# Kernel tuning notes

Measured on AMD Instinct MI355X. Metric: run time of the kernel, lower is better.

The kernel has to match this reference:

```python
import jax, jax.numpy as jnp
import numpy as np

B = 16
TOP_N = 4
IOU_THRESH = 0.25
PAD = 224
OUT = 224  # part image size
NUM_CLASSES = 200


def _gen_anchors(input_shape=(448, 448)):
    # Faithful port of NTSNet._generate_default_anchor_maps -> edge anchors,
    # then +PAD shift and int cast as in NTSNet.__init__.
    scales = [2.0 ** (1.0 / 3.0), 2.0 ** (2.0 / 3.0)]
    ratios = [0.667, 1.0, 1.5]
    settings = [(32, 48, scales), (64, 96, scales), (128, 192, [1.0] + scales)]
    edge = []
    for stride, size, scs in settings:
        H = int(np.ceil(input_shape[0] / stride))
        W = int(np.ceil(input_shape[1] / stride))
        ostart = stride / 2.0
        oy = np.arange(ostart, ostart + stride * H, stride).reshape(H, 1)
        ox = np.arange(ostart, ostart + stride * W, stride).reshape(1, W)
        cy = np.broadcast_to(oy, (H, W)).astype(np.float32)
        cx = np.broadcast_to(ox, (H, W)).astype(np.float32)
        for s in scs:
            for ar in ratios:
                h = size * s / float(ar) ** 0.5
                w = size * s * float(ar) ** 0.5
                e = np.stack([cy - h / 2.0, cx - w / 2.0, cy + h / 2.0, cx + w / 2.0], axis=-1)
                edge.append(e.reshape(-1, 4))
    edge = np.concatenate(edge, axis=0).astype(np.float32)
    return (edge + PAD).astype(np.int64).astype(np.int32)  # [1614,4] (y0,x0,y1,x1)


def _conv(x, w, b, stride, pad):
    y = jax.lax.conv_general_dilated(
        x, w, window_strides=(stride, stride),
        padding=[(pad, pad), (pad, pad)],
        dimension_numbers=("NCHW", "OIHW", "NCHW"))
    return y + b[None, :, None, None]


def _nms_single(scores, boxes, areas):
    # Hard NMS, fixed TOP_N iterations (jit-friendly): iteratively take the
    # highest-score box and suppress boxes with IoU >= IOU_THRESH.
    valid = jnp.ones(scores.shape, dtype=bool)
    picked = []
    for _ in range(TOP_N):
        i = jnp.argmax(jnp.where(valid, scores, -jnp.inf))
        b = boxes[i]
        ih = jnp.minimum(boxes[:, 2], b[2]) - jnp.maximum(boxes[:, 0], b[0])
        iw = jnp.minimum(boxes[:, 3], b[3]) - jnp.maximum(boxes[:, 1], b[1])
        inter = jnp.where((ih < 0) | (iw < 0), 0.0, ih * iw)
        iou = inter / (areas + areas[i] - inter)
        valid = valid & (iou < IOU_THRESH)
        picked.append(i)
    return jnp.stack(picked)  # [TOP_N]


def _crop_resize(img, box):
    # Bilinear resize of img[:, y0:y1, x0:x1] to OUTxOUT, align_corners=True
    # (matches F.interpolate(..., mode='bilinear', align_corners=True)).
    y0, x0, y1, x1 = box[0], box[1], box[2], box[3]
    h = (y1 - y0).astype(jnp.float32)
    w = (x1 - x0).astype(jnp.float32)
    t = jnp.arange(OUT, dtype=jnp.float32)
    sy = t * (h - 1.0) / (OUT - 1.0)
    sx = t * (w - 1.0) / (OUT - 1.0)
    fy = jnp.floor(sy)
    fx = jnp.floor(sx)
    wy = (sy - fy)[None, :, None]  # broadcast over rows
    wx = (sx - fx)[None, None, :]  # broadcast over cols
    iy0 = y0 + fy.astype(jnp.int32)
    ix0 = x0 + fx.astype(jnp.int32)
    iy1 = jnp.minimum(iy0 + 1, y1 - 1)
    ix1 = jnp.minimum(ix0 + 1, x1 - 1)
    r0 = img[:, iy0]  # [3,OUT,896]
    r1 = img[:, iy1]
    top = r0[:, :, ix0] * (1.0 - wx) + r0[:, :, ix1] * wx
    bot = r1[:, :, ix0] * (1.0 - wx) + r1[:, :, ix1] * wx
    return top * (1.0 - wy) + bot * wy  # [3,OUT,OUT]


def setup_inputs() -> dict:
    key = jax.random.key(0)
    ks = jax.random.split(key, 10)
    s = 0.02
    inp = {
        "x": jax.random.normal(ks[0], (B, 3, 448, 448), jnp.float32),
        "bb_w": jax.random.normal(ks[1], (2048, 3, 32, 32), jnp.float32) * s,
        "bb_b": jnp.zeros((2048,), jnp.float32),
        "n1_dw": jax.random.normal(ks[2], (128, 2048, 3, 3), jnp.float32) * s,
        "n1_db": jnp.zeros((128,), jnp.float32),
        "n1_tw": jax.random.normal(ks[3], (6, 128, 1, 1), jnp.float32) * s,
        "n1_tb": jnp.zeros((6,), jnp.float32),
        "n2_dw": jax.random.normal(ks[4], (128, 128, 3, 3), jnp.float32) * s,
        "n2_db": jnp.zeros((128,), jnp.float32),
        "n2_tw": jax.random.normal(ks[5], (6, 128, 1, 1), jnp.float32) * s,
        "n2_tb": jnp.zeros((6,), jnp.float32),
        "n3_dw": jax.random.normal(ks[6], (128, 128, 3, 3), jnp.float32) * s,
        "n3_db": jnp.zeros((128,), jnp.float32),
        "n3_tw": jax.random.normal(ks[7], (9, 128, 1, 1), jnp.float32) * s,
        "n3_tb": jnp.zeros((9,), jnp.float32),
        "cn_w": jax.random.normal(ks[8], (NUM_CLASSES, 10240), jnp.float32) * s,
        "cn_b": jnp.zeros((NUM_CLASSES,), jnp.float32),
        "anchors": jnp.asarray(_gen_anchors()),
    }
    return inp


def reference(x, bb_w, bb_b, n1_dw, n1_db, n1_tw, n1_tb, n2_dw, n2_db, n2_tw,
              n2_tb, n3_dw, n3_db, n3_tw, n3_tb, cn_w, cn_b, anchors):
    batch = x.shape[0]
    # Backbone -> raw pre-features [B,2048,14,14]
    raw = _conv(x, bb_w, bb_b, stride=32, pad=0)
    # Navigator unit -> rpn scores [B,1614]
    y1 = jax.nn.relu(_conv(raw, n1_dw, n1_db, 1, 1))            # [B,128,14,14]
    t1 = _conv(y1, n1_tw, n1_tb, 1, 0).reshape(batch, -1)        # [B,1176]
    y2 = jax.nn.relu(_conv(y1, n2_dw, n2_db, 2, 1))              # [B,128,7,7]
    t2 = _conv(y2, n2_tw, n2_tb, 1, 0).reshape(batch, -1)        # [B,294]
    y3 = jax.nn.relu(_conv(y2, n3_dw, n3_db, 2, 1))              # [B,128,4,4]
    t3 = _conv(y3, n3_tw, n3_tb, 1, 0).reshape(batch, -1)        # [B,144]
    rpn_score = jnp.concatenate([t1, t2, t3], axis=1)            # [B,1614]

    boxes_f = anchors.astype(jnp.float32)
    areas = (boxes_f[:, 2] - boxes_f[:, 0]) * (boxes_f[:, 3] - boxes_f[:, 1])
    top_idx = jax.vmap(_nms_single, in_axes=(0, None, None))(rpn_score, boxes_f, areas)  # [B,TOP_N]

    x_pad = jnp.pad(x, ((0, 0), (0, 0), (PAD, PAD), (PAD, PAD)))  # [B,3,896,896]
    sel_boxes = anchors[top_idx]                                  # [B,TOP_N,4]
    part_imgs = jax.vmap(lambda img, bs: jax.vmap(_crop_resize, in_axes=(None, 0))(img, bs))(
        x_pad, sel_boxes)                                         # [B,TOP_N,3,224,224]
    part_imgs = jax.lax.stop_gradient(part_imgs).reshape(batch * TOP_N, 3, OUT, OUT)

    # Shared backbone + tail (global avg pool; dropout is identity in eval)
    part_features = _conv(part_imgs, bb_w, bb_b, 32, 0).mean(axis=(2, 3))  # [B*TOP_N,2048]
    part_feature = part_features.reshape(batch, TOP_N, -1)[:, :4].reshape(batch, -1)  # num_cat=4
    raw_features = jax.lax.stop_gradient(raw).mean(axis=(2, 3))            # [B,2048]

    concat_out = jnp.concatenate([part_feature, raw_features], axis=1)     # [B,10240]
    concat_logits = concat_out @ cn_w.T + cn_b
    return concat_logits
```

## Files before the change

### kernel.cpp

```cpp
#include <hip/hip_runtime.h>
#include <cstdint>
#include <math.h>

typedef _Float16 half_t;
typedef __attribute__((ext_vector_type(8))) _Float16 half8;
typedef __attribute__((ext_vector_type(4))) float floatx4;


typedef __attribute__((address_space(3))) unsigned int lds_u32;
typedef const __attribute__((address_space(1))) unsigned int glb_u32;
__device__ __forceinline__ void glds16(const void* g, void* l) {
    __builtin_amdgcn_global_load_lds((glb_u32*)g, (lds_u32*)l, 16, 0, 0);
}

__global__ __launch_bounds__(256)
void prep_all(const float* __restrict__ x, const float* __restrict__ bbw,
              const float* __restrict__ n1dw, const float* __restrict__ n2dw,
              const float* __restrict__ n3dw, const float* __restrict__ cnb,
              const float* __restrict__ bbb,
              half_t* __restrict__ xh,
              half_t* __restrict__ bh, half_t* __restrict__ w1h,
              float* __restrict__ wt2t, float* __restrict__ wt3t,
              float* __restrict__ out, float* __restrict__ zpad,
              float* __restrict__ concat)
{
    const long t = (long)blockIdx.x * 256 + threadIdx.x;
    if (t < 1228800) {
        const int m = (int)(t % 3200), k8 = (int)(t / 3200);
        const int mt = m >> 7, mr = m & 127, s = k8 >> 2, kg = k8 & 3;
        const size_t dst = (((size_t)(mt * 96 + s) * 4 + kg) * 128 + mr) * 8;
        float f[8];
        if (m < 3136) {
            const int bq = m / 196, pos = m % 196, oy = pos / 14, ox = pos % 14;
            const int k = k8 * 8, c = k >> 10, r = (k >> 5) & 31, cc = k & 31;
            const float* p = x + ((size_t)(bq * 3 + c) * 448 + oy * 32 + r) * 448 + ox * 32 + cc;
            *(float4*)&f[0] = *(const float4*)p;
            *(float4*)&f[4] = *(const float4*)(p + 4);
        } else {
            #pragma unroll
            for (int j = 0; j < 8; ++j) f[j] = 0.f;
        }
        half8 h;
        #pragma unroll
        for (int j = 0; j < 8; ++j) h[j] = (half_t)f[j];
        *(half8*)(xh + dst) = h;
    } else if (t < 2015232) {
        const int t2 = (int)(t - 1228800);
        const int n = t2 / 384, k8 = t2 % 384;
        const float* p = bbw + (size_t)n * 3072 + k8 * 8;
        float f[8];
        *(float4*)&f[0] = *(const float4*)p;
        *(float4*)&f[4] = *(const float4*)(p + 4);
        const int nt = n >> 6, nr = n & 63, s = k8 >> 2, kg = k8 & 3;
        const size_t dst = (((size_t)(nt * 96 + s) * 4 + kg) * 64 + nr) * 8;
        half8 h;
        #pragma unroll
        for (int j = 0; j < 8; ++j) h[j] = (half_t)f[j];
        *(half8*)(bh + dst) = h;
    } else if (t < 2048000) {
        const int t2 = (int)(t - 2015232);
        const int n = t2 >> 8, ic8 = t2 & 255;
        const int s = ic8 >> 2, kg = ic8 & 3;
        const float* src = n1dw + ((size_t)n * 2048 + ic8 * 8) * 9;
        float buf[72];
        #pragma unroll
        for (int i = 0; i < 18; ++i) *(float4*)&buf[i * 4] = *(const float4*)(src + i * 4);
        #pragma unroll
        for (int tap = 0; tap < 9; ++tap) {
            half8 h;
            #pragma unroll
            for (int j = 0; j < 8; ++j) h[j] = (half_t)buf[j * 9 + tap];
            const size_t dst = (((size_t)(tap * 64 + s) * 4 + kg) * 128 + n) * 8;
            *(half8*)(w1h + dst) = h;
        }
    } else if (t < 2195456) {
        const int t2 = (int)(t - 2048000);
        const int oc = t2 % 128, rest = t2 / 128, ic = rest % 128, tap = rest / 128;
        wt2t[(tap * 128 + ic) * 128 + oc] = n2dw[((size_t)oc * 128 + ic) * 9 + tap];
    } else if (t < 2342912) {
        const int t2 = (int)(t - 2195456);
        const int oc = t2 % 128, rest = t2 / 128, ic = rest % 128, tap = rest / 128;
        wt3t[(tap * 128 + ic) * 128 + oc] = n3dw[((size_t)oc * 128 + ic) * 9 + tap];
    } else if (t < 2346112) {
        const int i = (int)(t - 2342912);
        out[i] = cnb[i % 200];
    } else if (t < 2346368) {
        zpad[t - 2346112] = 0.f;
    } else if (t < 2510208) {
        const int i = (int)(t - 2346368);
        const int r = i % 10240;
        concat[i] = (r < 8192) ? bbb[r & 2047] : 0.f;
    }
}

__global__ __launch_bounds__(256)
void gemm_x(const half_t* __restrict__ Ah, const half_t* __restrict__ Bh,
            const float* __restrict__ bias, half_t* __restrict__ outh)
{
    __shared__ __align__(16) char L[24576];
    const int tid = threadIdx.x, lane = tid & 63, wv = tid >> 6;
    const int nt = blockIdx.x, mt = blockIdx.y;
    const int lm = lane & 15, quad = lane >> 4;

    const char* gA = (const char*)Ah + (size_t)(mt >> 1) * 786432 + (mt & 1) * 1024 + lane * 16;
    const char* gB = (const char*)Bh + (size_t)(2 * nt) * 393216 + lane * 16;

    const int a0 = 2 * wv, a1 = 2 * wv + 1;
    const int aof0 = (a0 >> 2) * 4096 + (a0 & 3) * 1024;
    const int aog0 = (a0 >> 2) * 8192 + (a0 & 3) * 2048;
    const int aof1 = (a1 >> 2) * 4096 + (a1 & 3) * 1024;
    const int aog1 = (a1 >> 2) * 8192 + (a1 & 3) * 2048;
    const int bsi = wv >> 1, bnh = wv & 1;
    const size_t bgb = (size_t)bnh * 393216 + bsi * 4096;
    const int blb = 8192 + (bsi * 2 + bnh) * 4096;

    floatx4 acc[8];
    const floatx4 fz = {0.f, 0.f, 0.f, 0.f};
    #pragma unroll
    for (int j = 0; j < 8; ++j) acc[j] = fz;

    for (int s = 0; s < 48; ++s) {
        const size_t sa = (size_t)(2 * s) * 8192;
        const size_t sb = (size_t)(2 * s) * 4096;
        glds16(gA + sa + aog0, L + aof0);
        glds16(gA + sa + aog1, L + aof1);
        #pragma unroll
        for (int i = 0; i < 4; ++i)
            glds16(gB + bgb + sb + i * 1024, L + blb + i * 1024);
        __syncthreads();
        #pragma unroll
        for (int ki = 0; ki < 2; ++ki) {
            half8 a = *(const half8*)(L + ki * 4096 + quad * 1024 + (wv * 16 + lm) * 16);
            #pragma unroll
            for (int j = 0; j < 8; ++j) {
                half8 b = *(const half8*)(L + 8192 + (ki * 2 + (j >> 2)) * 4096 + quad * 1024 + ((j & 3) * 16 + lm) * 16);
                acc[j] = __builtin_amdgcn_mfma_f32_16x16x32_f16(a, b, acc[j], 0, 0, 0);
            }
        }
        __syncthreads();
    }
    const int m0 = mt * 64 + wv * 16 + quad * 4;
    #pragma unroll
    for (int j = 0; j < 8; ++j) {
        const int n = nt * 128 + j * 16 + lm;
        const float bv = bias[n];
        #pragma unroll
        for (int r = 0; r < 4; ++r)
            outh[(size_t)(m0 + r) * 2048 + n] = (half_t)(acc[j][r] + bv);
    }
}

__global__ __launch_bounds__(256)
void gemm_nav(const half_t* __restrict__ rawh, const half_t* __restrict__ Bh,
              const char* __restrict__ zpad, float* __restrict__ y1p)
{
    __shared__ __align__(16) char L[24576];
    const int tid = threadIdx.x, lane = tid & 63, wv = tid >> 6;
    const int tx = blockIdx.x;
    const int tap = tx >> 1, ks = tx & 1;
    const int mt = blockIdx.y;
    const int lm = lane & 15, quad = lane >> 4;

    const int grow = mt * 64 + lane;
    const int b = grow / 196, pos = grow % 196, oy = pos / 14, ox = pos % 14;
    const int iy = oy + tap / 3 - 1, ix = ox + tap % 3 - 1;
    const bool av = (iy >= 0 && iy < 14 && ix >= 0 && ix < 14);
    const char* abase = av ? (const char*)rawh + ((size_t)(b * 196 + iy * 14 + ix)) * 4096 + ks * 2048 : zpad;
    const int stp = av ? 1 : 0;

    const int a0 = 2 * wv, a1 = 2 * wv + 1;
    const int ac0 = (a0 >> 2) * 64 + (a0 & 3) * 16, al0 = (a0 >> 2) * 4096 + (a0 & 3) * 1024;
    const int ac1 = (a1 >> 2) * 64 + (a1 & 3) * 16, al1 = (a1 >> 2) * 4096 + (a1 & 3) * 1024;
    const int bsi = wv >> 1, bnh = wv & 1;
    const char* gB = (const char*)Bh + (size_t)tap * 524288 + (size_t)(ks * 32) * 8192 + bnh * 1024 + lane * 16;
    const int blb = 8192 + bsi * 8192 + bnh * 1024;

    floatx4 acc[8];
    const floatx4 fz = {0.f, 0.f, 0.f, 0.f};
    #pragma unroll
    for (int j = 0; j < 8; ++j) acc[j] = fz;

    for (int s = 0; s < 16; ++s) {
        const int rowo = s * 128;
        glds16(abase + stp * (rowo + ac0), L + al0);
        glds16(abase + stp * (rowo + ac1), L + al1);
        const size_t sb = (size_t)(2 * s + bsi) * 8192;
        #pragma unroll
        for (int i = 0; i < 4; ++i)
            glds16(gB + sb + i * 2048, L + blb + i * 2048);
        __syncthreads();
        #pragma unroll
        for (int ki = 0; ki < 2; ++ki) {
            half8 a = *(const half8*)(L + ki * 4096 + quad * 1024 + (wv * 16 + lm) * 16);
            #pragma unroll
            for (int j = 0; j < 8; ++j) {
                half8 bq = *(const half8*)(L + 8192 + ki * 8192 + quad * 2048 + (j * 16 + lm) * 16);
                acc[j] = __builtin_amdgcn_mfma_f32_16x16x32_f16(a, bq, acc[j], 0, 0, 0);
            }
        }
        __syncthreads();
    }
    const int m0 = mt * 64 + wv * 16 + quad * 4;
    #pragma unroll
    for (int j = 0; j < 8; ++j) {
        const int n = j * 16 + lm;
        #pragma unroll
        for (int r = 0; r < 4; ++r)
            y1p[((size_t)tx * 3136 + m0 + r) * 128 + n] = acc[j][r];
    }
}

__global__ __launch_bounds__(256)
void y1r_rm(const float* __restrict__ y1p, const float* __restrict__ bias,
            float* __restrict__ y1,
            const half_t* __restrict__ rh, float* __restrict__ concat)
{
    if (blockIdx.x < 1568) {
        const int t = blockIdx.x * 256 + threadIdx.x;
        const int n = t & 127;
        float s = bias[n];
        #pragma unroll
        for (int ks = 0; ks < 18; ++ks) s += y1p[(size_t)ks * 3136 * 128 + t];
        y1[t] = fmaxf(s, 0.f);
    } else {
        const int t = (blockIdx.x - 1568) * 256 + threadIdx.x;
        const int n = t & 2047, b = (t >> 11) & 15, pc = t >> 15;
        float s = 0.f;
        const int p0 = pc * 49;
        for (int p = p0; p < p0 + 49; ++p)
            s += (float)rh[(size_t)(b * 196 + p) * 2048 + n];
        atomicAdd(concat + (size_t)b * 10240 + 8192 + n, s * (1.f / 196.f));
    }
}

__device__ __forceinline__ void tidy_one(const float* in, const float* wr, float bi,
                                         float* dst, int lane)
{
    float acc = in[lane] * wr[lane] + in[lane + 64] * wr[lane + 64];
    #pragma unroll
    for (int s = 32; s > 0; s >>= 1) acc += __shfl_down(acc, s, 64);
    if (lane == 0) *dst = acc + bi;
}

__device__ __forceinline__ void conv_s2_body(int t, const float* __restrict__ in,
                                             const float* __restrict__ wt,
                                             const float* __restrict__ bias,
                                             float* __restrict__ out, int Win, int Wout)
{
    const int oc = t & 127;
    const int pos = (t >> 7) % (Wout * Wout);
    const int b = t / (128 * Wout * Wout);
    if (b >= 16) return;
    const int oy = pos / Wout, ox = pos % Wout;
    float acc = bias[oc];
    for (int dy = 0; dy < 3; ++dy) {
        const int y = oy * 2 + dy - 1;
        if (y < 0 || y >= Win) continue;
        for (int dx = 0; dx < 3; ++dx) {
            const int x = ox * 2 + dx - 1;
            if (x < 0 || x >= Win) continue;
            const float* ip = in + (size_t)(b * Win * Win + y * Win + x) * 128;
            const float* wp = wt + (size_t)(dy * 3 + dx) * 16384 + oc;
            for (int ic = 0; ic < 128; ++ic)
                acc += ip[ic] * wp[ic * 128];
        }
    }
    out[(size_t)(b * Wout * Wout + pos) * 128 + oc] = fmaxf(acc, 0.f);
}

__global__ __launch_bounds__(256)
void conv2_tidy1(const float* __restrict__ y1, const float* __restrict__ wt2t,
                 const float* __restrict__ b2d, float* __restrict__ y2,
                 const float* __restrict__ w1t, const float* __restrict__ b1t,
                 float* __restrict__ scores)
{
    if (blockIdx.x < 392) {
        conv_s2_body(blockIdx.x * 256 + threadIdx.x, y1, wt2t, b2d, y2, 14, 7);
    } else {
        const int wid = (blockIdx.x - 392) * 4 + (threadIdx.x >> 6);
        const int lane = threadIdx.x & 63;
        if (wid >= 16 * 1176) return;
        const int b = wid / 1176, i1 = wid % 1176;
        const int ch = i1 / 196, pos = i1 % 196;
        tidy_one(y1 + (size_t)(b * 196 + pos) * 128, w1t + ch * 128, b1t[ch],
                 scores + b * 1614 + i1, lane);
    }
}

__global__ __launch_bounds__(256)
void conv3_tidy2(const float* __restrict__ y2, const float* __restrict__ wt3t,
                 const float* __restrict__ b3d, float* __restrict__ y3,
                 const float* __restrict__ w2t, const float* __restrict__ b2t,
                 float* __restrict__ scores)
{
    if (blockIdx.x < 128) {
        conv_s2_body(blockIdx.x * 256 + threadIdx.x, y2, wt3t, b3d, y3, 7, 4);
    } else {
        const int wid = (blockIdx.x - 128) * 4 + (threadIdx.x >> 6);
        const int lane = threadIdx.x & 63;
        if (wid >= 16 * 294) return;
        const int b = wid / 294, i2 = wid % 294;
        const int ch = i2 / 49, pos = i2 % 49;
        tidy_one(y2 + (size_t)(b * 49 + pos) * 128, w2t + ch * 128, b2t[ch],
                 scores + b * 1614 + 1176 + i2, lane);
    }
}

__global__ __launch_bounds__(256)
void tidy3(const float* __restrict__ y3, const float* __restrict__ w3t,
           const float* __restrict__ b3t, float* __restrict__ scores)
{
    const int wid = blockIdx.x * 4 + (threadIdx.x >> 6);
    const int lane = threadIdx.x & 63;
    if (wid >= 16 * 144) return;
    const int b = wid / 144, i3 = wid % 144;
    const int ch = i3 / 16, pos = i3 % 16;
    tidy_one(y3 + (size_t)(b * 16 + pos) * 128, w3t + ch * 128, b3t[ch],
             scores + b * 1614 + 1470 + i3, lane);
}

__global__ __launch_bounds__(256)
void nms(const float* __restrict__ scores, const int* __restrict__ anchors,
         int* __restrict__ top_idx)
{
    __shared__ float wv_v[4];
    __shared__ int wv_i[4];
    __shared__ int s_pick;
    const int b = blockIdx.x, tid = threadIdx.x;
    const int lane = tid & 63, wv = tid >> 6;
    float sc[7], ay0[7], ax0[7], ay1[7], ax1[7];
    unsigned int vmask = 0;
    #pragma unroll
    for (int j = 0; j < 7; ++j) {
        const int i = tid + j * 256;
        if (i < 1614) {
            sc[j]  = scores[b * 1614 + i];
            ay0[j] = (float)anchors[i * 4 + 0];
            ax0[j] = (float)anchors[i * 4 + 1];
            ay1[j] = (float)anchors[i * 4 + 2];
            ax1[j] = (float)anchors[i * 4 + 3];
            vmask |= 1u << j;
        }
    }
    for (int r = 0; r < 4; ++r) {
        float bv = -INFINITY; int bi = 0x7fffffff;
        #pragma unroll
        for (int j = 0; j < 7; ++j) {
            if (vmask & (1u << j)) {
                const float v = sc[j];
                const int i = tid + j * 256;
                if (v > bv || (v == bv && i < bi)) { bv = v; bi = i; }
            }
        }
        #pragma unroll
        for (int s = 32; s > 0; s >>= 1) {
            const float v2 = __shfl_down(bv, s, 64);
            const int   i2 = __shfl_down(bi, s, 64);
            if (v2 > bv || (v2 == bv && i2 < bi)) { bv = v2; bi = i2; }
        }
        if (lane == 0) { wv_v[wv] = bv; wv_i[wv] = bi; }
        __syncthreads();
        if (tid == 0) {
            float fv = wv_v[0]; int fi = wv_i[0];
            #pragma unroll
            for (int k = 1; k < 4; ++k)
                if (wv_v[k] > fv || (wv_v[k] == fv && wv_i[k] < fi)) { fv = wv_v[k]; fi = wv_i[k]; }
            s_pick = fi;
            top_idx[b * 4 + r] = fi;
        }
        __syncthreads();
        const int pick = s_pick;
        const float py0 = (float)anchors[pick * 4 + 0], px0 = (float)anchors[pick * 4 + 1];
        const float py1 = (float)anchors[pick * 4 + 2], px1 = (float)anchors[pick * 4 + 3];
        const float pa = (py1 - py0) * (px1 - px0);
        #pragma unroll
        for (int j = 0; j < 7; ++j) {
            if (vmask & (1u << j)) {
                const float ih = fminf(ay1[j], py1) - fmaxf(ay0[j], py0);
                const float iw = fminf(ax1[j], px1) - fmaxf(ax0[j], px0);
                const float inter = (ih < 0.f || iw < 0.f) ? 0.f : ih * iw;
                const float area = (ay1[j] - ay0[j]) * (ax1[j] - ax0[j]);
                const float iou = inter / ((area + pa) - inter);
                if (iou >= 0.25f) vmask &= ~(1u << j);
            }
        }
    }
}

__global__ __launch_bounds__(256)
void crop_mean(const float* __restrict__ x, const int* __restrict__ anchors,
               const int* __restrict__ top_idx, float* __restrict__ abar)
{
    __shared__ float red[256];
    const int bi = blockIdx.x;
    const int q = bi / 96, rem = bi % 96, c = rem >> 5, r = rem & 31;
    const int tid = threadIdx.x;
    const int cc = tid & 31, ps = tid >> 5;
    const int idx = top_idx[q];
    const int y0 = anchors[idx * 4 + 0], x0 = anchors[idx * 4 + 1];
    const int y1 = anchors[idx * 4 + 2], x1 = anchors[idx * 4 + 3];
    const float hh = (float)(y1 - y0), ww = (float)(x1 - x0);
    const float* xb = x + (size_t)((q >> 2) * 3 + c) * 200704;
    float acc = 0.f;
    for (int p = ps; p < 49; p += 8) {
        const int oy = p / 7, ox = p % 7;
        const int typ = oy * 32 + r;
        const int txp = ox * 32 + cc;
        const float sy = (float)typ * (hh - 1.0f) / 223.0f;
        const float fy = floorf(sy);
        const float wy = sy - fy;
        const int iy0 = y0 + (int)fy;
        const int iy1 = min(iy0 + 1, y1 - 1);
        const float sx = (float)txp * (ww - 1.0f) / 223.0f;
        const float fx = floorf(sx);
        const float wx = sx - fx;
        const int ix0 = x0 + (int)fx;
        const int ix1 = min(ix0 + 1, x1 - 1);
        const int ry0 = iy0 - 224, ry1 = iy1 - 224;
        const int rx0 = ix0 - 224, rx1 = ix1 - 224;
        const bool vy0 = (ry0 >= 0 && ry0 < 448), vy1 = (ry1 >= 0 && ry1 < 448);
        const bool vx0 = (rx0 >= 0 && rx0 < 448), vx1 = (rx1 >= 0 && rx1 < 448);
        const float v00 = (vy0 && vx0) ? xb[(size_t)ry0 * 448 + rx0] : 0.f;
        const float v01 = (vy0 && vx1) ? xb[(size_t)ry0 * 448 + rx1] : 0.f;
        const float v10 = (vy1 && vx0) ? xb[(size_t)ry1 * 448 + rx0] : 0.f;
        const float v11 = (vy1 && vx1) ? xb[(size_t)ry1 * 448 + rx1] : 0.f;
        const float top = v00 * (1.f - wx) + v01 * wx;
        const float bot = v10 * (1.f - wx) + v11 * wx;
        acc += top * (1.f - wy) + bot * wy;
    }
    red[tid] = acc;
    __syncthreads();
    if (tid < 32) {
        float s = 0.f;
        #pragma unroll
        for (int k = 0; k < 8; ++k) s += red[tid + 32 * k];
        abar[(size_t)q * 3072 + c * 1024 + r * 32 + cc] = s * (1.f / 49.f);
    }
}

__global__ __launch_bounds__(256)
void part_gemm(const float* __restrict__ abar, const half_t* __restrict__ Bh,
               float* __restrict__ concat)
{
    __shared__ __align__(16) char L[12288];
    const int tid = threadIdx.x, lane = tid & 63, wv = tid >> 6;
    const int lm = lane & 15, quad = lane >> 4;
    const int nt = blockIdx.x, ks = blockIdx.y;
    const char* gBh = (const char*)Bh + ((size_t)nt * 96 + ks * 12) * 4096 + lane * 16;
    const int am = tid & 63, akg = tid >> 6;

    floatx4 acc[4], accl[4];
    const floatx4 fz = {0.f, 0.f, 0.f, 0.f};
    #pragma unroll
    for (int j = 0; j < 4; ++j) { acc[j] = fz; accl[j] = fz; }

    for (int s = 0; s < 12; ++s) {
        {
            const float* pa = abar + (size_t)am * 3072 + (ks * 12 + s) * 32 + akg * 8;
            float f[8];
            *(float4*)&f[0] = *(const float4*)pa;
            *(float4*)&f[4] = *(const float4*)(pa + 4);
            half8 h, l;
            #pragma unroll
            for (int j = 0; j < 8; ++j) {
                const half_t hh = (half_t)f[j];
                h[j] = hh;
                l[j] = (half_t)(f[j] - (float)hh);
            }
            *(half8*)(L + (akg * 64 + am) * 16) = h;
            *(half8*)(L + 4096 + (akg * 64 + am) * 16) = l;
        }
        glds16(gBh + (size_t)s * 4096 + wv * 1024, L + 8192 + wv * 1024);
        __syncthreads();
        half8 ah, al, bh[4];
        ah = *(const half8*)(L + (quad * 64 + wv * 16 + lm) * 16);
        al = *(const half8*)(L + 4096 + (quad * 64 + wv * 16 + lm) * 16);
        #pragma unroll
        for (int j = 0; j < 4; ++j) bh[j] = *(const half8*)(L + 8192 + (quad * 64 + j * 16 + lm) * 16);
        #pragma unroll
        for (int j = 0; j < 4; ++j) {
            acc[j]  = __builtin_amdgcn_mfma_f32_16x16x32_f16(ah, bh[j], acc[j], 0, 0, 0);
            accl[j] = __builtin_amdgcn_mfma_f32_16x16x32_f16(al, bh[j], accl[j], 0, 0, 0);
        }
        __syncthreads();
    }
    #pragma unroll
    for (int j = 0; j < 4; ++j) {
        const int n = nt * 64 + j * 16 + lm;
        #pragma unroll
        for (int r = 0; r < 4; ++r) {
            const int m = wv * 16 + quad * 4 + r;
            atomicAdd(concat + (size_t)(m >> 2) * 10240 + (m & 3) * 2048 + n,
                      acc[j][r] + accl[j][r]);
        }
    }
}

__global__ __launch_bounds__(256)
void cls_gemm(const float* __restrict__ concat, const float* __restrict__ w,
              float* __restrict__ out)
{
    __shared__ float ws_[8 * 321];
    __shared__ float cs_[16 * 321];
    __shared__ float red[256];
    const int nchunk = blockIdx.x, ks = blockIdx.y;
    const int tid = threadIdx.x;
    for (int i = tid; i < 2560; i += 256) {
        const int r = i / 320, k = i % 320;
        ws_[r * 321 + k] = w[(size_t)(nchunk * 8 + r) * 10240 + ks * 320 + k];
    }
    for (int i = tid; i < 5120; i += 256) {
        const int r = i / 320, k = i % 320;
        cs_[r * 321 + k] = concat[(size_t)r * 10240 + ks * 320 + k];
    }
    __syncthreads();
    const int b = tid & 15, c = (tid >> 4) & 7, hf = tid >> 7;
    const float* cp = cs_ + b * 321 + hf * 160;
    const float* wp = ws_ + c * 321 + hf * 160;
    float a = 0.f;
    #pragma unroll 8
    for (int k = 0; k < 160; ++k) a += cp[k] * wp[k];
    red[tid] = a;
    __syncthreads();
    if (tid < 128) atomicAdd(out + b * 200 + nchunk * 8 + c, red[tid] + red[tid + 128]);
}

extern "C" void kernel_launch(void* const* d_in, const int* in_sizes, int n_in,
                              void* d_out, int out_size, void* d_ws, size_t ws_size,
                              hipStream_t stream)
{
    const float* x     = (const float*)d_in[0];
    const float* bb_w  = (const float*)d_in[1];
    const float* bb_b  = (const float*)d_in[2];
    const float* n1_dw = (const float*)d_in[3];
    const float* n1_db = (const float*)d_in[4];
    const float* n1_tw = (const float*)d_in[5];
    const float* n1_tb = (const float*)d_in[6];
    const float* n2_dw = (const float*)d_in[7];
    const float* n2_db = (const float*)d_in[8];
    const float* n2_tw = (const float*)d_in[9];
    const float* n2_tb = (const float*)d_in[10];
    const float* n3_dw = (const float*)d_in[11];
    const float* n3_db = (const float*)d_in[12];
    const float* n3_tw = (const float*)d_in[13];
    const float* n3_tb = (const float*)d_in[14];
    const float* cn_w  = (const float*)d_in[15];
    const float* cn_b  = (const float*)d_in[16];
    const int*   anchors = (const int*)d_in[17];
    float* out = (float*)d_out;
    char* W = (char*)d_ws;

    half_t* bbwh  = (half_t*)(W + 0);
    float*  zpad  = (float*)(W + 12582912);
    int*    topidx= (int*)(W + 12583936);
    float*  scores= (float*)(W + 12584960);
    float*  y1    = (float*)(W + 12688384);
    float*  y2    = (float*)(W + 14294016);
    float*  y3    = (float*)(W + 14695424);
    float*  concat= (float*)(W + 14826496);
    half_t* w1h   = (half_t*)(W + 15481856);
    float*  wt2t  = (float*)(W + 20200448);
    float*  wt3t  = (float*)(W + 20790272);
    char* E = W + 21380096;
    half_t* xh    = (half_t*)E;
    float*  y1p   = (float*)E;
    char* F = W + 60701696;
    half_t* rawh  = (half_t*)F;
    float*  abar  = (float*)F;

    prep_all<<<9806, 256, 0, stream>>>(x, bb_w, n1_dw, n2_dw, n3_dw, cn_b, bb_b,
                                       xh, bbwh, w1h, wt2t, wt3t, out, zpad, concat);

    gemm_x<<<dim3(16, 49), 256, 0, stream>>>(xh, bbwh, bb_b, rawh);
    gemm_nav<<<dim3(18, 49), 256, 0, stream>>>(rawh, w1h, (const char*)zpad, y1p);
    y1r_rm<<<2080, 256, 0, stream>>>(y1p, n1_db, y1, rawh, concat);

    conv2_tidy1<<<5096, 256, 0, stream>>>(y1, wt2t, n2_db, y2, n1_tw, n1_tb, scores);
    conv3_tidy2<<<1304, 256, 0, stream>>>(y2, wt3t, n3_db, y3, n2_tw, n2_tb, scores);
    tidy3<<<576, 256, 0, stream>>>(y3, n3_tw, n3_tb, scores);

    nms<<<16, 256, 0, stream>>>(scores, anchors, topidx);
    crop_mean<<<6144, 256, 0, stream>>>(x, anchors, topidx, abar);

    part_gemm<<<dim3(32, 8), 256, 0, stream>>>(abar, bbwh, concat);
    cls_gemm<<<dim3(25, 32), 256, 0, stream>>>(concat, cn_w, out);
}
```

Before: 396.0 us.

## Double-buffer LDS in GEMMs, swizzle blocks across XCDs, coarsen prep threads

gemm_x and gemm_nav now double-buffer their shared-memory tiles. The next k-step's global-to-LDS loads are issued before the MFMA work on the current buffer, and each step ends with a single waitcnt plus barrier, so load latency overlaps compute. Both kernels also remap block indices so neighbouring tiles land on the same XCD, which should improve L2 reuse. prep_all has each thread convert 32 elements instead of 8 for the input and backbone weights, cutting the grid size. The trade-off is twice the LDS per block, which may lower occupancy.

```diff
diff --git a/kernel.cpp b/kernel.cpp
--- a/kernel.cpp
+++ b/kernel.cpp
@@ -24,41 +24,47 @@
               float* __restrict__ out, float* __restrict__ zpad,
               float* __restrict__ concat)
 {
-    const long t = (long)blockIdx.x * 256 + threadIdx.x;
-    if (t < 1228800) {
-        const int m = (int)(t % 3200), k8 = (int)(t / 3200);
-        const int mt = m >> 7, mr = m & 127, s = k8 >> 2, kg = k8 & 3;
-        const size_t dst = (((size_t)(mt * 96 + s) * 4 + kg) * 128 + mr) * 8;
-        float f[8];
+    const int t = blockIdx.x * 256 + threadIdx.x;
+    if (t < 307200) {
+        const int m = t % 3200, s = t / 3200;
+        const int mt = m >> 7, mr = m & 127;
+        float f[32];
         if (m < 3136) {
             const int bq = m / 196, pos = m % 196, oy = pos / 14, ox = pos % 14;
-            const int k = k8 * 8, c = k >> 10, r = (k >> 5) & 31, cc = k & 31;
-            const float* p = x + ((size_t)(bq * 3 + c) * 448 + oy * 32 + r) * 448 + ox * 32 + cc;
-            *(float4*)&f[0] = *(const float4*)p;
-            *(float4*)&f[4] = *(const float4*)(p + 4);
+            const int c = s >> 5, r = s & 31;
+            const float* p = x + ((size_t)(bq * 3 + c) * 448 + oy * 32 + r) * 448 + ox * 32;
+            #pragma unroll
+            for (int i = 0; i < 8; ++i) *(float4*)&f[i * 4] = *(const float4*)(p + i * 4);
         } else {
             #pragma unroll
-            for (int j = 0; j < 8; ++j) f[j] = 0.f;
-        }
-        half8 h;
-        #pragma unroll
-        for (int j = 0; j < 8; ++j) h[j] = (half_t)f[j];
-        *(half8*)(xh + dst) = h;
-    } else if (t < 2015232) {
-        const int t2 = (int)(t - 1228800);
-        const int n = t2 / 384, k8 = t2 % 384;
-        const float* p = bbw + (size_t)n * 3072 + k8 * 8;
-        float f[8];
-        *(float4*)&f[0] = *(const float4*)p;
-        *(float4*)&f[4] = *(const float4*)(p + 4);
-        const int nt = n >> 6, nr = n & 63, s = k8 >> 2, kg = k8 & 3;
-        const size_t dst = (((size_t)(nt * 96 + s) * 4 + kg) * 64 + nr) * 8;
-        half8 h;
-        #pragma unroll
-        for (int j = 0; j < 8; ++j) h[j] = (half_t)f[j];
-        *(half8*)(bh + dst) = h;
-    } else if (t < 2048000) {
-        const int t2 = (int)(t - 2015232);
+            for (int j = 0; j < 32; ++j) f[j] = 0.f;
+        }
+        #pragma unroll
+        for (int kg = 0; kg < 4; ++kg) {
+            half8 h;
+            #pragma unroll
+            for (int j = 0; j < 8; ++j) h[j] = (half_t)f[kg * 8 + j];
+            const size_t dst = (((size_t)(mt * 96 + s) * 4 + kg) * 128 + mr) * 8;
+            *(half8*)(xh + dst) = h;
+        }
+    } else if (t < 503808) {
+        const int t2 = t - 307200;
+        const int n = t2 & 2047, s = t2 >> 11;
+        const float* p = bbw + (size_t)n * 3072 + s * 32;
+        float f[32];
+        #pragma unroll
+        for (int i = 0; i < 8; ++i) *(float4*)&f[i * 4] = *(const float4*)(p + i * 4);
+        const int nt = n >> 6, nr = n & 63;
+        #pragma unroll
+        for (int kg = 0; kg < 4; ++kg) {
+            half8 h;
+            #pragma unroll
+            for (int j = 0; j < 8; ++j) h[j] = (half_t)f[kg * 8 + j];
+            const size_t dst = (((size_t)(nt * 96 + s) * 4 + kg) * 64 + nr) * 8;
+            *(half8*)(bh + dst) = h;
+        }
+    } else if (t < 536576) {
+        const int t2 = t - 503808;
         const int n = t2 >> 8, ic8 = t2 & 255;
         const int s = ic8 >> 2, kg = ic8 & 3;
         const float* src = n1dw + ((size_t)n * 2048 + ic8 * 8) * 9;
@@ -73,21 +79,21 @@
             const size_t dst = (((size_t)(tap * 64 + s) * 4 + kg) * 128 + n) * 8;
             *(half8*)(w1h + dst) = h;
         }
-    } else if (t < 2195456) {
-        const int t2 = (int)(t - 2048000);
+    } else if (t < 684032) {
+        const int t2 = t - 536576;
         const int oc = t2 % 128, rest = t2 / 128, ic = rest % 128, tap = rest / 128;
         wt2t[(tap * 128 + ic) * 128 + oc] = n2dw[((size_t)oc * 128 + ic) * 9 + tap];
-    } else if (t < 2342912) {
-        const int t2 = (int)(t - 2195456);
+    } else if (t < 831488) {
+        const int t2 = t - 684032;
         const int oc = t2 % 128, rest = t2 / 128, ic = rest % 128, tap = rest / 128;
         wt3t[(tap * 128 + ic) * 128 + oc] = n3dw[((size_t)oc * 128 + ic) * 9 + tap];
-    } else if (t < 2346112) {
-        const int i = (int)(t - 2342912);
+    } else if (t < 834688) {
+        const int i = t - 831488;
         out[i] = cnb[i % 200];
-    } else if (t < 2346368) {
-        zpad[t - 2346112] = 0.f;
-    } else if (t < 2510208) {
-        const int i = (int)(t - 2346368);
+    } else if (t < 834944) {
+        zpad[t - 834688] = 0.f;
+    } else if (t < 998784) {
+        const int i = t - 834944;
         const int r = i % 10240;
         concat[i] = (r < 8192) ? bbb[r & 2047] : 0.f;
     }
@@ -97,9 +103,11 @@
 void gemm_x(const half_t* __restrict__ Ah, const half_t* __restrict__ Bh,
             const float* __restrict__ bias, half_t* __restrict__ outh)
 {
-    __shared__ __align__(16) char L[24576];
+    __shared__ __align__(16) char L[49152];
     const int tid = threadIdx.x, lane = tid & 63, wv = tid >> 6;
-    const int nt = blockIdx.x, mt = blockIdx.y;
+    const int bid = blockIdx.y * 16 + blockIdx.x;
+    const int swz = (bid & 7) * 98 + (bid >> 3);
+    const int nt = swz & 15, mt = swz >> 4;
     const int lm = lane & 15, quad = lane >> 4;
 
     const char* gA = (const char*)Ah + (size_t)(mt >> 1) * 786432 + (mt & 1) * 1024 + lane * 16;
@@ -119,25 +127,37 @@
     #pragma unroll
     for (int j = 0; j < 8; ++j) acc[j] = fz;
 
+    glds16(gA + aog0, L + aof0);
+    glds16(gA + aog1, L + aof1);
+    #pragma unroll
+    for (int i = 0; i < 4; ++i)
+        glds16(gB + bgb + i * 1024, L + blb + i * 1024);
+    asm volatile("s_waitcnt vmcnt(0)" ::: "memory");
+    __builtin_amdgcn_s_barrier();
+
     for (int s = 0; s < 48; ++s) {
-        const size_t sa = (size_t)(2 * s) * 8192;
-        const size_t sb = (size_t)(2 * s) * 4096;
-        glds16(gA + sa + aog0, L + aof0);
-        glds16(gA + sa + aog1, L + aof1);
-        #pragma unroll
-        for (int i = 0; i < 4; ++i)
-            glds16(gB + bgb + sb + i * 1024, L + blb + i * 1024);
-        __syncthreads();
+        const char* Lc = L + (s & 1) * 24576;
+        char* Ln = L + ((s + 1) & 1) * 24576;
+        if (s < 47) {
+            const size_t sa = (size_t)(2 * (s + 1)) * 8192;
+            const size_t sb = (size_t)(2 * (s + 1)) * 4096;
+            glds16(gA + sa + aog0, Ln + aof0);
+            glds16(gA + sa + aog1, Ln + aof1);
+            #pragma unroll
+            for (int i = 0; i < 4; ++i)
+                glds16(gB + bgb + sb + i * 1024, Ln + blb + i * 1024);
+        }
         #pragma unroll
         for (int ki = 0; ki < 2; ++ki) {
-            half8 a = *(const half8*)(L + ki * 4096 + quad * 1024 + (wv * 16 + lm) * 16);
+            half8 a = *(const half8*)(Lc + ki * 4096 + quad * 1024 + (wv * 16 + lm) * 16);
             #pragma unroll
             for (int j = 0; j < 8; ++j) {
-                half8 b = *(const half8*)(L + 8192 + (ki * 2 + (j >> 2)) * 4096 + quad * 1024 + ((j & 3) * 16 + lm) * 16);
+                half8 b = *(const half8*)(Lc + 8192 + (ki * 2 + (j >> 2)) * 4096 + quad * 1024 + ((j & 3) * 16 + lm) * 16);
                 acc[j] = __builtin_amdgcn_mfma_f32_16x16x32_f16(a, b, acc[j], 0, 0, 0);
             }
         }
-        __syncthreads();
+        asm volatile("s_waitcnt vmcnt(0) lgkmcnt(0)" ::: "memory");
+        __builtin_amdgcn_s_barrier();
     }
     const int m0 = mt * 64 + wv * 16 + quad * 4;
     #pragma unroll
@@ -154,11 +174,13 @@
 void gemm_nav(const half_t* __restrict__ rawh, const half_t* __restrict__ Bh,
               const char* __restrict__ zpad, float* __restrict__ y1p)
 {
-    __shared__ __align__(16) char L[24576];
+    __shared__ __align__(16) char L[49152];
     const int tid = threadIdx.x, lane = tid & 63, wv = tid >> 6;
-    const int tx = blockIdx.x;
+    const int bid = blockIdx.y * 18 + blockIdx.x;
+    const int xcd = bid & 7, ii = bid >> 3;
+    const int swz = (xcd < 2 ? xcd * 111 : 222 + (xcd - 2) * 110) + ii;
+    const int tx = swz % 18, mt = swz / 18;
     const int tap = tx >> 1, ks = tx & 1;
-    const int mt = blockIdx.y;
     const int lm = lane & 15, quad = lane >> 4;
 
     const int grow = mt * 64 + lane;
@@ -180,25 +202,40 @@
     #pragma unroll
     for (int j = 0; j < 8; ++j) acc[j] = fz;
 
+    glds16(abase + stp * ac0, L + al0);
+    glds16(abase + stp * ac1, L + al1);
+    {
+        const size_t sb0 = (size_t)bsi * 8192;
+        #pragma unroll
+        for (int i = 0; i < 4; ++i)
+            glds16(gB + sb0 + i * 2048, L + blb + i * 2048);
+    }
+    asm volatile("s_waitcnt vmcnt(0)" ::: "memory");
+    __builtin_amdgcn_s_barrier();
+
     for (int s = 0; s < 16; ++s) {
-        const int rowo = s * 128;
-        glds16(abase + stp * (rowo + ac0), L + al0);
-        glds16(abase + stp * (rowo + ac1), L + al1);
-        const size_t sb = (size_t)(2 * s + bsi) * 8192;
-        #pragma unroll
-        for (int i = 0; i < 4; ++i)
-            glds16(gB + sb + i * 2048, L + blb + i * 2048);
-        __syncthreads();
+        const char* Lc = L + (s & 1) * 24576;
+        char* Ln = L + ((s + 1) & 1) * 24576;
+        if (s < 15) {
+            const int rowo = (s + 1) * 128;
+            glds16(abase + stp * (rowo + ac0), Ln + al0);
+            glds16(abase + stp * (rowo + ac1), Ln + al1);
+            const size_t sb = (size_t)(2 * (s + 1) + bsi) * 8192;
+            #pragma unroll
+            for (int i = 0; i < 4; ++i)
+                glds16(gB + sb + i * 2048, Ln + blb + i * 2048);
+        }
         #pragma unroll
         for (int ki = 0; ki < 2; ++ki) {
-            half8 a = *(const half8*)(L + ki * 4096 + quad * 1024 + (wv * 16 + lm) * 16);
+            half8 a = *(const half8*)(Lc + ki * 4096 + quad * 1024 + (wv * 16 + lm) * 16);
             #pragma unroll
             for (int j = 0; j < 8; ++j) {
-                half8 bq = *(const half8*)(L + 8192 + ki * 8192 + quad * 2048 + (j * 16 + lm) * 16);
+                half8 bq = *(const half8*)(Lc + 8192 + ki * 8192 + quad * 2048 + (j * 16 + lm) * 16);
                 acc[j] = __builtin_amdgcn_mfma_f32_16x16x32_f16(a, bq, acc[j], 0, 0, 0);
             }
         }
-        __syncthreads();
+        asm volatile("s_waitcnt vmcnt(0) lgkmcnt(0)" ::: "memory");
+        __builtin_amdgcn_s_barrier();
     }
     const int m0 = mt * 64 + wv * 16 + quad * 4;
     #pragma unroll
@@ -568,7 +605,7 @@
     half_t* rawh  = (half_t*)F;
     float*  abar  = (float*)F;
 
-    prep_all<<<9806, 256, 0, stream>>>(x, bb_w, n1_dw, n2_dw, n3_dw, cn_b, bb_b,
+    prep_all<<<3902, 256, 0, stream>>>(x, bb_w, n1_dw, n2_dw, n3_dw, cn_b, bb_b,
                                        xh, bbwh, w1h, wt2t, wt3t, out, zpad, concat);
 
     gemm_x<<<dim3(16, 49), 256, 0, stream>>>(xh, bbwh, bb_b, rawh);
```

New measurement: 400.8 us. No clear change (+1.2%).
